# Kernel optimization log

Measured on AMD Instinct MI355X. Metric: run time of the kernel, lower is better.

The kernel has to match this reference:

```python
import jax, jax.numpy as jnp
import numpy as np

B, T, D, H, R = 16, 2048, 512, 1024, 16


def setup_inputs() -> dict:
    key = jax.random.key(0)
    ks = jax.random.split(key, 8)
    s = lambda d: 1.0 / np.sqrt(d)
    return {
        "x": jax.random.normal(ks[0], (B, T, D), jnp.float32),
        "Wx": jax.random.normal(ks[1], (D, H), jnp.float32) * s(D),
        "Wh": jax.random.normal(ks[2], (H, H), jnp.float32) * s(H),
        "Wq": jax.random.normal(ks[3], (D, R), jnp.float32) * s(D),
        "Wk": jax.random.normal(ks[4], (D, R), jnp.float32) * s(D),
        "Wv": jax.random.normal(ks[5], (D, H), jnp.float32) * s(D),
        "Wd": jax.random.normal(ks[6], (D, 1), jnp.float32) * s(D),
        "b": jnp.zeros((H,), jnp.float32),
        "bd": jnp.ones((1,), jnp.float32),
    }


def reference(x, Wx, Wh, Wq, Wk, Wv, Wd, b, bd):
    """DREAM fast-weight RNN.

    Per step: decay lambda_t = sigmoid(x_t Wd + bd)  (B,1)
              F_t = lambda_t * F_{t-1} + v_t k_t^T   (B,H,R) outer-product memory
              r_t = F_t q_t                          (B,H)   fast-weight read
              h_t = tanh(x_t Wx + h_{t-1} Wh + r_t + b)
    """
    Bsz = x.shape[0]
    Hd, Rk = Wv.shape[1], Wq.shape[1]
    # Precompute all time-parallel projections once (big GEMMs outside the scan).
    q = jnp.einsum('btd,dr->btr', x, Wq)            # (B,T,R)
    k = jnp.einsum('btd,dr->btr', x, Wk)            # (B,T,R)
    v = jnp.einsum('btd,dh->bth', x, Wv)            # (B,T,H)
    lam = jax.nn.sigmoid(jnp.einsum('btd,do->bto', x, Wd) + bd)  # (B,T,1)
    xw = jnp.einsum('btd,dh->bth', x, Wx)           # (B,T,H)

    h0 = jnp.zeros((Bsz, Hd), x.dtype)
    F0 = jnp.zeros((Bsz, Hd, Rk), x.dtype)

    def step(carry, inp):
        h, F = carry
        q_t, k_t, v_t, lam_t, xw_t = inp
        F = lam_t[:, :, None] * F + v_t[:, :, None] * k_t[:, None, :]  # (B,H,R)
        read = jnp.einsum('bhr,br->bh', F, q_t)
        h = jnp.tanh(xw_t + h @ Wh + read + b)
        return (h, F), h

    # scan over time axis
    inps = (q.transpose(1, 0, 2), k.transpose(1, 0, 2), v.transpose(1, 0, 2),
            lam.transpose(1, 0, 2), xw.transpose(1, 0, 2))
    (h_fin, F_fin), hs = jax.lax.scan(step, (h0, F0), inps)
    output = hs.transpose(1, 0, 2)  # (B,T,H)
    return output, h_fin, F_fin
```

## Files before the change

### kernel.cpp

```cpp
#include <hip/hip_runtime.h>
#include <math.h>

#define Bc 16
#define Tc 2048
#define Dc 512
#define Hc 1024
#define Rc 16

__global__ __launch_bounds__(256) void proj_fused(const float* __restrict__ X,
    const float* __restrict__ Wx, const float* __restrict__ Wv,
    const float* __restrict__ Wq, const float* __restrict__ Wk,
    const float* __restrict__ Wd, const float* __restrict__ bd,
    float* __restrict__ out0, float* __restrict__ vout,
    float* __restrict__ q, float* __restrict__ k, float* __restrict__ lam)
{
    __shared__ float smem[8192];
    const int tid = threadIdx.x;

    if (blockIdx.z < 2) {
        float (*As)[128] = (float (*)[128])smem;
        float (*Bs)[128] = (float (*)[128])(smem + 2048);
        const float* W = blockIdx.z ? Wv : Wx;
        float* out     = blockIdx.z ? vout : out0;
        const int m0 = blockIdx.x * 128;
        const int n0 = blockIdx.y * 128;
        const int tx = tid & 15, ty = tid >> 4;
        const int ar = tid >> 1, ak = (tid & 1) * 8;
        const int br = tid >> 4, bn = (tid & 15) * 8;
        float acc[8][8] = {};
        for (int k0 = 0; k0 < 512; k0 += 16) {
            if (k0) __syncthreads();
            float4 a0 = *(const float4*)&X[(size_t)(m0 + ar) * 512 + k0 + ak];
            float4 a1 = *(const float4*)&X[(size_t)(m0 + ar) * 512 + k0 + ak + 4];
            float4 b0 = *(const float4*)&W[(size_t)(k0 + br) * 1024 + n0 + bn];
            float4 b1 = *(const float4*)&W[(size_t)(k0 + br) * 1024 + n0 + bn + 4];
            As[ak + 0][ar] = a0.x; As[ak + 1][ar] = a0.y;
            As[ak + 2][ar] = a0.z; As[ak + 3][ar] = a0.w;
            As[ak + 4][ar] = a1.x; As[ak + 5][ar] = a1.y;
            As[ak + 6][ar] = a1.z; As[ak + 7][ar] = a1.w;
            *(float4*)&Bs[br][bn]     = b0;
            *(float4*)&Bs[br][bn + 4] = b1;
            __syncthreads();
            #pragma unroll
            for (int kk = 0; kk < 16; ++kk) {
                float4 xa = *(const float4*)&As[kk][ty * 8];
                float4 xb = *(const float4*)&As[kk][ty * 8 + 4];
                float4 ya = *(const float4*)&Bs[kk][tx * 8];
                float4 yb = *(const float4*)&Bs[kk][tx * 8 + 4];
                float a[8] = {xa.x, xa.y, xa.z, xa.w, xb.x, xb.y, xb.z, xb.w};
                float b[8] = {ya.x, ya.y, ya.z, ya.w, yb.x, yb.y, yb.z, yb.w};
                #pragma unroll
                for (int i = 0; i < 8; ++i)
                    #pragma unroll
                    for (int j = 0; j < 8; ++j)
                        acc[i][j] += a[i] * b[j];
            }
        }
        #pragma unroll
        for (int i = 0; i < 8; ++i) {
            float4 r0, r1;
            r0.x = acc[i][0]; r0.y = acc[i][1]; r0.z = acc[i][2]; r0.w = acc[i][3];
            r1.x = acc[i][4]; r1.y = acc[i][5]; r1.z = acc[i][6]; r1.w = acc[i][7];
            float* op = &out[(size_t)(m0 + ty * 8 + i) * 1024 + n0 + tx * 8];
            *(float4*)op       = r0;
            *(float4*)(op + 4) = r1;
        }
    } else {
        float* xs = smem;
        const int rb = blockIdx.x * 8 + blockIdx.y;
        const size_t row0 = (size_t)rb * 16;
        #pragma unroll
        for (int c = 0; c < 8; ++c) {
            int f = (c * 256 + tid) * 4;
            *(float4*)&xs[f] = *(const float4*)&X[row0 * 512 + f];
        }
        __syncthreads();
        for (int t = tid; t < 528; t += 256) {
            int r = t / 33, c = t - r * 33;
            const float* xr = &xs[r * 512];
            const float* Wp; int ldw;
            if (c < 16)      { Wp = Wq + c;        ldw = 16; }
            else if (c < 32) { Wp = Wk + (c - 16); ldw = 16; }
            else             { Wp = Wd;            ldw = 1;  }
            float s = 0.f;
            for (int kk = 0; kk < 512; ++kk) s += xr[kk] * Wp[(size_t)kk * ldw];
            if (c < 16)      q[(row0 + r) * 16 + c] = s;
            else if (c < 32) k[(row0 + r) * 16 + (c - 16)] = s;
            else             lam[row0 + r] = 1.f / (1.f + expf(-(s + bd[0])));
        }
    }
}

__global__ __launch_bounds__(256, 1) void rec_fused(
    const float* __restrict__ Wh, const float* __restrict__ qg,
    const float* __restrict__ kg, const float* __restrict__ vg,
    const float* __restrict__ lamg, const float* __restrict__ bias,
    float* __restrict__ out0, float* __restrict__ hfin,
    float* __restrict__ Ffin, float* __restrict__ hbuf,
    int* __restrict__ xcc_tab)
{
    __shared__ float hs[2 * 1152];
    __shared__ float red2[2][256];
    __shared__ float pre_lds[2][64];
    __shared__ float F_lds[64][17];

    const int tid = threadIdx.x;
    const int bid = blockIdx.x;
    const int g = bid & 7, sl = bid >> 3;
    const int c0 = sl * 32;
    const int kp = tid >> 3;
    const int cu = tid & 7;
    const int wv = tid >> 6;

    const int my_xcc = __builtin_amdgcn_s_getreg(63508) & 0xF;
    if (tid == 0) {
        int val = my_xcc + 1;
        int* tp = xcc_tab + bid;
        asm volatile("global_store_dword %0, %1, off sc0 sc1"
                     :: "v"(tp), "v"(val) : "memory");
    }

    float wr[128];
    #pragma unroll
    for (int i = 0; i < 32; ++i) {
        float4 w4 = *(const float4*)&Wh[(size_t)(kp * 32 + i) * 1024 + c0 + cu * 4];
        wr[i * 4 + 0] = w4.x; wr[i * 4 + 1] = w4.y;
        wr[i * 4 + 2] = w4.z; wr[i * 4 + 3] = w4.w;
    }

    const int sb_ = tid >> 7;
    const int f   = (tid & 127) * 8;
    float* stage_base = &hs[sb_ * 1152 + (f >> 5) * 36 + (f & 31)];

    int fastf;
    {
        const int prod_bid = (f >> 5) * 8 + g;
        const int* tp = xcc_tab + prod_bid;
        int tv;
        for (;;) {
            asm volatile("global_load_dword %0, %1, off sc0 sc1\n\t"
                         "s_waitcnt vmcnt(0)"
                         : "=&v"(tv) : "v"(tp) : "memory");
            if (tv != -1) break;
        }
        fastf = ((tv - 1) == my_xcc) ? 1 : 0;
    }

    const int j64 = tid & 63;
    const int fb = j64 >> 5, fci = j64 & 31;
    const int bg = g * 2 + fb;
    const bool isScan = (tid >= 192);
    const bool isFin  = (tid < 64);

    float bias_r = 0.f, plam = 0.f, pv = 0.f, pxw = 0.f;
    float4 pq[4], pk4[4];
    if (isScan) {
        bias_r = bias[c0 + fci];
        #pragma unroll
        for (int r = 0; r < 16; ++r) F_lds[j64][r] = 0.f;
        const size_t row = (size_t)bg * Tc;
        plam = lamg[row];
        pv   = vg[row * Hc + c0 + fci];
        pxw  = out0[row * Hc + c0 + fci];
        const float* qp  = qg + row * 16;
        const float* kpp = kg + row * 16;
        #pragma unroll
        for (int r4 = 0; r4 < 4; ++r4) {
            pq[r4]  = *(const float4*)(qp + r4 * 4);
            pk4[r4] = *(const float4*)(kpp + r4 * 4);
        }
    }

    for (int t = 0; t < Tc; ++t) {
        const int buf = t & 1;
        float* h_rd = hbuf + (t & 1) * (16 * 1024) + g * 2048;
        float* h_wr = hbuf + ((t + 1) & 1) * (16 * 1024) + g * 2048;
        const float off_r = ((t >> 1) & 1) ? 4.0f : 0.0f;
        const float off_w = (((t + 1) >> 1) & 1) ? 4.0f : 0.0f;

        if (isScan) {
            float rd = 0.f;
            #pragma unroll
            for (int r4 = 0; r4 < 4; ++r4) {
                float f0 = F_lds[j64][r4 * 4 + 0];
                float f1 = F_lds[j64][r4 * 4 + 1];
                float f2 = F_lds[j64][r4 * 4 + 2];
                float f3 = F_lds[j64][r4 * 4 + 3];
                f0 = plam * f0 + pv * pk4[r4].x; rd += f0 * pq[r4].x;
                f1 = plam * f1 + pv * pk4[r4].y; rd += f1 * pq[r4].y;
                f2 = plam * f2 + pv * pk4[r4].z; rd += f2 * pq[r4].z;
                f3 = plam * f3 + pv * pk4[r4].w; rd += f3 * pq[r4].w;
                F_lds[j64][r4 * 4 + 0] = f0;
                F_lds[j64][r4 * 4 + 1] = f1;
                F_lds[j64][r4 * 4 + 2] = f2;
                F_lds[j64][r4 * 4 + 3] = f3;
            }
            pre_lds[buf][j64] = pxw + rd + bias_r;
            if (t == Tc - 1) {
                #pragma unroll
                for (int r = 0; r < 16; ++r)
                    Ffin[((size_t)bg * Hc + c0 + fci) * 16 + r] = F_lds[j64][r];
            } else {
                const size_t row = (size_t)bg * Tc + (t + 1);
                plam = lamg[row];
                pv   = vg[row * Hc + c0 + fci];
                pxw  = out0[row * Hc + c0 + fci];
                const float* qp  = qg + row * 16;
                const float* kpp = kg + row * 16;
                #pragma unroll
                for (int r4 = 0; r4 < 4; ++r4) {
                    pq[r4]  = *(const float4*)(qp + r4 * 4);
                    pk4[r4] = *(const float4*)(kpp + r4 * 4);
                }
            }
        }

        if (t > 0) {
            const float lo = off_r - 1.5f, hi = off_r + 1.5f;
            const float* p0 = h_rd + sb_ * 1024 + f;
            const float* p1 = p0 + 4;
            float4 r0, r1;
            int tries = 0;
            for (;;) {
                if (fastf) {
                    asm volatile(
                        "global_load_dwordx4 %0, %2, off sc0\n\t"
                        "global_load_dwordx4 %1, %3, off sc0\n\t"
                        "s_waitcnt vmcnt(0)"
                        : "=&v"(r0), "=&v"(r1)
                        : "v"(p0), "v"(p1) : "memory");
                } else {
                    asm volatile(
                        "global_load_dwordx4 %0, %2, off sc0 sc1\n\t"
                        "global_load_dwordx4 %1, %3, off sc0 sc1\n\t"
                        "s_waitcnt vmcnt(0)"
                        : "=&v"(r0), "=&v"(r1)
                        : "v"(p0), "v"(p1) : "memory");
                }
                bool ok = r0.x > lo && r0.x < hi && r0.y > lo && r0.y < hi
                       && r0.z > lo && r0.z < hi && r0.w > lo && r0.w < hi
                       && r1.x > lo && r1.x < hi && r1.y > lo && r1.y < hi
                       && r1.z > lo && r1.z < hi && r1.w > lo && r1.w < hi;
                if (ok) break;
                if (fastf && ++tries > 64) fastf = 0;
            }
            r0.x -= off_r; r0.y -= off_r; r0.z -= off_r; r0.w -= off_r;
            r1.x -= off_r; r1.y -= off_r; r1.z -= off_r; r1.w -= off_r;
            *(float4*)(stage_base)     = r0;
            *(float4*)(stage_base + 4) = r1;
        } else {
            float4 z = {0.f, 0.f, 0.f, 0.f};
            *(float4*)(stage_base)     = z;
            *(float4*)(stage_base + 4) = z;
        }
        __syncthreads();

        float acc[8];
        #pragma unroll
        for (int z = 0; z < 8; ++z) acc[z] = 0.f;
        #pragma unroll
        for (int bb = 0; bb < 2; ++bb) {
            const float* hb = &hs[bb * 1152 + kp * 36];
            #pragma unroll
            for (int i = 0; i < 8; ++i) {
                float4 h4 = *(const float4*)(hb + i * 4);
                #pragma unroll
                for (int j = 0; j < 4; ++j)
                    acc[j * 2 + bb] += h4.x * wr[(i * 4 + 0) * 4 + j]
                                     + h4.y * wr[(i * 4 + 1) * 4 + j]
                                     + h4.z * wr[(i * 4 + 2) * 4 + j]
                                     + h4.w * wr[(i * 4 + 3) * 4 + j];
            }
        }

        #pragma unroll
        for (int z = 0; z < 8; ++z) {
            float s = acc[z];
            s += __shfl_xor(s, 8);
            s += __shfl_xor(s, 16);
            s += __shfl_xor(s, 32);
            acc[z] = s;
        }
        if (j64 < 8) {
            float4 ra, rb;
            ra.x = acc[0]; ra.y = acc[1]; ra.z = acc[2]; ra.w = acc[3];
            rb.x = acc[4]; rb.y = acc[5]; rb.z = acc[6]; rb.w = acc[7];
            *(float4*)&red2[buf][wv * 64 + j64 * 8]     = ra;
            *(float4*)&red2[buf][wv * 64 + j64 * 8 + 4] = rb;
        }
        __syncthreads();

        if (isFin) {
            const int cu_f = fci >> 2, jf = fci & 3;
            const int z = jf * 2 + fb;
            float tot = pre_lds[buf][j64];
            #pragma unroll
            for (int ww = 0; ww < 4; ++ww)
                tot += red2[buf][ww * 64 + cu_f * 8 + z];
            float hv = tanhf(tot);
            float sv = hv + off_w;
            float* hp = h_wr + fb * 1024 + c0 + fci;
            asm volatile(
                "global_store_dword %0, %1, off sc0 sc1"
                :: "v"(hp), "v"(sv) : "memory");
            size_t oidx = ((size_t)bg * Tc + t) * Hc + c0 + fci;
            out0[oidx] = hv;
            if (t == Tc - 1) hfin[(size_t)bg * Hc + c0 + fci] = hv;
        }
    }
}

extern "C" void kernel_launch(void* const* d_in, const int* in_sizes, int n_in,
                              void* d_out, int out_size, void* d_ws, size_t ws_size,
                              hipStream_t stream)
{
    const float* x    = (const float*)d_in[0];
    const float* Wx   = (const float*)d_in[1];
    const float* Wh   = (const float*)d_in[2];
    const float* Wq   = (const float*)d_in[3];
    const float* Wk   = (const float*)d_in[4];
    const float* Wv   = (const float*)d_in[5];
    const float* Wd   = (const float*)d_in[6];
    const float* bias = (const float*)d_in[7];
    const float* bd   = (const float*)d_in[8];

    float* out0 = (float*)d_out;
    float* hfin = out0 + (size_t)Bc * Tc * Hc;
    float* Ffin = hfin + (size_t)Bc * Hc;

    float* wsf  = (float*)d_ws;
    float* v    = wsf;
    float* q    = v + (size_t)Bc * Tc * Hc;
    float* k    = q + (size_t)Bc * Tc * Rc;
    float* lam  = k + (size_t)Bc * Tc * Rc;
    float* hbuf = lam + (size_t)Bc * Tc;
    int*   xcc  = (int*)(hbuf + 2 * (size_t)Bc * Hc);

    hipMemsetAsync(hbuf, 0x7F, 2 * (size_t)Bc * Hc * sizeof(float), stream);
    hipMemsetAsync(xcc, 0xFF, 256 * sizeof(int), stream);

    dim3 gp(256, 8, 3);
    proj_fused<<<gp, 256, 0, stream>>>(x, Wx, Wv, Wq, Wk, Wd, bd,
                                       out0, v, q, k, lam);
    rec_fused<<<256, 256, 0, stream>>>(Wh, q, k, v, lam, bias,
                                       out0, hfin, Ffin, hbuf, xcc);
}
```

Measured before the change: 7.519 ms.

## Fuse projection and recurrence into one persistent kernel with readiness flags

Merges the projection GEMM kernel and the recurrent scan kernel into a single launch. The first 256 blocks run the recurrence, and the remaining blocks compute the projections, publishing per-tile ready flags. Recurrence threads spin on these flags before consuming each 128-step or 16-row chunk, so the scan can start while later projection tiles are still being computed. This removes the launch gap and lets the serial recurrence overlap the GEMM. The risks are deadlock if the recurrence blocks are not all co-resident, less register headroom from launch_bounds(256,2) for the weight-in-register recurrence, and polling overhead.

```diff
diff --git a/kernel.cpp b/kernel.cpp
--- a/kernel.cpp
+++ b/kernel.cpp
@@ -7,105 +7,124 @@
 #define Hc 1024
 #define Rc 16
 
-__global__ __launch_bounds__(256) void proj_fused(const float* __restrict__ X,
+__global__ __launch_bounds__(256, 2) void mega(
+    const float* __restrict__ X,
     const float* __restrict__ Wx, const float* __restrict__ Wv,
     const float* __restrict__ Wq, const float* __restrict__ Wk,
     const float* __restrict__ Wd, const float* __restrict__ bd,
-    float* __restrict__ out0, float* __restrict__ vout,
-    float* __restrict__ q, float* __restrict__ k, float* __restrict__ lam)
+    const float* __restrict__ Wh, const float* __restrict__ bias,
+    float* __restrict__ out0, float* __restrict__ hfin,
+    float* __restrict__ Ffin,
+    float* __restrict__ vg, float* __restrict__ qg, float* __restrict__ kg,
+    float* __restrict__ lamg, float* __restrict__ hbuf,
+    int* __restrict__ xcc_tab,
+    int* __restrict__ fxw, int* __restrict__ fv, int* __restrict__ fqkl)
 {
     __shared__ float smem[8192];
     const int tid = threadIdx.x;
-
-    if (blockIdx.z < 2) {
-        float (*As)[128] = (float (*)[128])smem;
-        float (*Bs)[128] = (float (*)[128])(smem + 2048);
-        const float* W = blockIdx.z ? Wv : Wx;
-        float* out     = blockIdx.z ? vout : out0;
-        const int m0 = blockIdx.x * 128;
-        const int n0 = blockIdx.y * 128;
-        const int tx = tid & 15, ty = tid >> 4;
-        const int ar = tid >> 1, ak = (tid & 1) * 8;
-        const int br = tid >> 4, bn = (tid & 15) * 8;
-        float acc[8][8] = {};
-        for (int k0 = 0; k0 < 512; k0 += 16) {
-            if (k0) __syncthreads();
-            float4 a0 = *(const float4*)&X[(size_t)(m0 + ar) * 512 + k0 + ak];
-            float4 a1 = *(const float4*)&X[(size_t)(m0 + ar) * 512 + k0 + ak + 4];
-            float4 b0 = *(const float4*)&W[(size_t)(k0 + br) * 1024 + n0 + bn];
-            float4 b1 = *(const float4*)&W[(size_t)(k0 + br) * 1024 + n0 + bn + 4];
-            As[ak + 0][ar] = a0.x; As[ak + 1][ar] = a0.y;
-            As[ak + 2][ar] = a0.z; As[ak + 3][ar] = a0.w;
-            As[ak + 4][ar] = a1.x; As[ak + 5][ar] = a1.y;
-            As[ak + 6][ar] = a1.z; As[ak + 7][ar] = a1.w;
-            *(float4*)&Bs[br][bn]     = b0;
-            *(float4*)&Bs[br][bn + 4] = b1;
+    const int bid = blockIdx.x;
+
+    if (bid >= 256) {
+        const int pb = bid - 256;
+        if (pb < 4096) {
+            const int which = pb >> 11;
+            const int idx = pb & 2047;
+            const int mblk = idx >> 3, nblk = idx & 7;
+            float (*As)[128] = (float (*)[128])smem;
+            float (*Bs)[128] = (float (*)[128])(smem + 2048);
+            const float* W = which ? Wv : Wx;
+            float* out     = which ? vg : out0;
+            const int m0 = mblk * 128;
+            const int n0 = nblk * 128;
+            const int tx = tid & 15, ty = tid >> 4;
+            const int ar = tid >> 1, ak = (tid & 1) * 8;
+            const int br = tid >> 4, bn = (tid & 15) * 8;
+            float acc[8][8] = {};
+            for (int k0 = 0; k0 < 512; k0 += 16) {
+                if (k0) __syncthreads();
+                float4 a0 = *(const float4*)&X[(size_t)(m0 + ar) * 512 + k0 + ak];
+                float4 a1 = *(const float4*)&X[(size_t)(m0 + ar) * 512 + k0 + ak + 4];
+                float4 b0 = *(const float4*)&W[(size_t)(k0 + br) * 1024 + n0 + bn];
+                float4 b1 = *(const float4*)&W[(size_t)(k0 + br) * 1024 + n0 + bn + 4];
+                As[ak + 0][ar] = a0.x; As[ak + 1][ar] = a0.y;
+                As[ak + 2][ar] = a0.z; As[ak + 3][ar] = a0.w;
+                As[ak + 4][ar] = a1.x; As[ak + 5][ar] = a1.y;
+                As[ak + 6][ar] = a1.z; As[ak + 7][ar] = a1.w;
+                *(float4*)&Bs[br][bn]     = b0;
+                *(float4*)&Bs[br][bn + 4] = b1;
+                __syncthreads();
+                #pragma unroll
+                for (int kk = 0; kk < 16; ++kk) {
+                    float4 xa = *(const float4*)&As[kk][ty * 8];
+                    float4 xb = *(const float4*)&As[kk][ty * 8 + 4];
+                    float4 ya = *(const float4*)&Bs[kk][tx * 8];
+                    float4 yb = *(const float4*)&Bs[kk][tx * 8 + 4];
+                    float a[8] = {xa.x, xa.y, xa.z, xa.w, xb.x, xb.y, xb.z, xb.w};
+                    float b[8] = {ya.x, ya.y, ya.z, ya.w, yb.x, yb.y, yb.z, yb.w};
+                    #pragma unroll
+                    for (int i = 0; i < 8; ++i)
+                        #pragma unroll
+                        for (int j = 0; j < 8; ++j)
+                            acc[i][j] += a[i] * b[j];
+                }
+            }
+            #pragma unroll
+            for (int i = 0; i < 8; ++i) {
+                float4 r0, r1;
+                r0.x = acc[i][0]; r0.y = acc[i][1]; r0.z = acc[i][2]; r0.w = acc[i][3];
+                r1.x = acc[i][4]; r1.y = acc[i][5]; r1.z = acc[i][6]; r1.w = acc[i][7];
+                float* op = &out[(size_t)(m0 + ty * 8 + i) * 1024 + n0 + tx * 8];
+                *(float4*)op       = r0;
+                *(float4*)(op + 4) = r1;
+            }
             __syncthreads();
+            if (tid == 0) {
+                __builtin_amdgcn_fence(__ATOMIC_RELEASE, "agent");
+                int one = 1;
+                int* fp = (which ? fv : fxw) + idx;
+                asm volatile("global_store_dword %0, %1, off sc0 sc1"
+                             :: "v"(fp), "v"(one) : "memory");
+            }
+        } else {
+            const int rb = pb - 4096;
+            float* xs = smem;
+            const size_t row0 = (size_t)rb * 16;
             #pragma unroll
-            for (int kk = 0; kk < 16; ++kk) {
-                float4 xa = *(const float4*)&As[kk][ty * 8];
-                float4 xb = *(const float4*)&As[kk][ty * 8 + 4];
-                float4 ya = *(const float4*)&Bs[kk][tx * 8];
-                float4 yb = *(const float4*)&Bs[kk][tx * 8 + 4];
-                float a[8] = {xa.x, xa.y, xa.z, xa.w, xb.x, xb.y, xb.z, xb.w};
-                float b[8] = {ya.x, ya.y, ya.z, ya.w, yb.x, yb.y, yb.z, yb.w};
-                #pragma unroll
-                for (int i = 0; i < 8; ++i)
-                    #pragma unroll
-                    for (int j = 0; j < 8; ++j)
-                        acc[i][j] += a[i] * b[j];
-            }
-        }
-        #pragma unroll
-        for (int i = 0; i < 8; ++i) {
-            float4 r0, r1;
-            r0.x = acc[i][0]; r0.y = acc[i][1]; r0.z = acc[i][2]; r0.w = acc[i][3];
-            r1.x = acc[i][4]; r1.y = acc[i][5]; r1.z = acc[i][6]; r1.w = acc[i][7];
-            float* op = &out[(size_t)(m0 + ty * 8 + i) * 1024 + n0 + tx * 8];
-            *(float4*)op       = r0;
-            *(float4*)(op + 4) = r1;
-        }
-    } else {
-        float* xs = smem;
-        const int rb = blockIdx.x * 8 + blockIdx.y;
-        const size_t row0 = (size_t)rb * 16;
-        #pragma unroll
-        for (int c = 0; c < 8; ++c) {
-            int f = (c * 256 + tid) * 4;
-            *(float4*)&xs[f] = *(const float4*)&X[row0 * 512 + f];
-        }
-        __syncthreads();
-        for (int t = tid; t < 528; t += 256) {
-            int r = t / 33, c = t - r * 33;
-            const float* xr = &xs[r * 512];
-            const float* Wp; int ldw;
-            if (c < 16)      { Wp = Wq + c;        ldw = 16; }
-            else if (c < 32) { Wp = Wk + (c - 16); ldw = 16; }
-            else             { Wp = Wd;            ldw = 1;  }
-            float s = 0.f;
-            for (int kk = 0; kk < 512; ++kk) s += xr[kk] * Wp[(size_t)kk * ldw];
-            if (c < 16)      q[(row0 + r) * 16 + c] = s;
-            else if (c < 32) k[(row0 + r) * 16 + (c - 16)] = s;
-            else             lam[row0 + r] = 1.f / (1.f + expf(-(s + bd[0])));
-        }
-    }
-}
-
-__global__ __launch_bounds__(256, 1) void rec_fused(
-    const float* __restrict__ Wh, const float* __restrict__ qg,
-    const float* __restrict__ kg, const float* __restrict__ vg,
-    const float* __restrict__ lamg, const float* __restrict__ bias,
-    float* __restrict__ out0, float* __restrict__ hfin,
-    float* __restrict__ Ffin, float* __restrict__ hbuf,
-    int* __restrict__ xcc_tab)
-{
-    __shared__ float hs[2 * 1152];
-    __shared__ float red2[2][256];
-    __shared__ float pre_lds[2][64];
-    __shared__ float F_lds[64][17];
-
-    const int tid = threadIdx.x;
-    const int bid = blockIdx.x;
+            for (int c = 0; c < 8; ++c) {
+                int f = (c * 256 + tid) * 4;
+                *(float4*)&xs[f] = *(const float4*)&X[row0 * 512 + f];
+            }
+            __syncthreads();
+            for (int t = tid; t < 528; t += 256) {
+                int r = t / 33, c = t - r * 33;
+                const float* xr = &xs[r * 512];
+                const float* Wp; int ldw;
+                if (c < 16)      { Wp = Wq + c;        ldw = 16; }
+                else if (c < 32) { Wp = Wk + (c - 16); ldw = 16; }
+                else             { Wp = Wd;            ldw = 1;  }
+                float s = 0.f;
+                for (int kk = 0; kk < 512; ++kk) s += xr[kk] * Wp[(size_t)kk * ldw];
+                if (c < 16)      qg[(row0 + r) * 16 + c] = s;
+                else if (c < 32) kg[(row0 + r) * 16 + (c - 16)] = s;
+                else             lamg[row0 + r] = 1.f / (1.f + expf(-(s + bd[0])));
+            }
+            __syncthreads();
+            if (tid == 0) {
+                __builtin_amdgcn_fence(__ATOMIC_RELEASE, "agent");
+                int one = 1;
+                int* fp = fqkl + rb;
+                asm volatile("global_store_dword %0, %1, off sc0 sc1"
+                             :: "v"(fp), "v"(one) : "memory");
+            }
+        }
+        return;
+    }
+
+    float* hs       = smem;
+    float* red2     = smem + 2304;
+    float* pre_lds  = smem + 2816;
+    float (*F_lds)[17] = (float (*)[17])(smem + 2944);
+
     const int g = bid & 7, sl = bid >> 3;
     const int c0 = sl * 32;
     const int kp = tid >> 3;
@@ -158,6 +177,31 @@
         bias_r = bias[c0 + fci];
         #pragma unroll
         for (int r = 0; r < 16; ++r) F_lds[j64][r] = 0.f;
+        {
+            const int fidx = (bg * 16 + 0) * 8 + (sl >> 2);
+            int fvv;
+            const int* fp1 = fxw + fidx;
+            for (;;) {
+                asm volatile("global_load_dword %0, %1, off sc0 sc1\n\t"
+                             "s_waitcnt vmcnt(0)" : "=&v"(fvv) : "v"(fp1) : "memory");
+                if (fvv) break;
+                __builtin_amdgcn_s_sleep(8);
+            }
+            const int* fp2 = fv + fidx;
+            for (;;) {
+                asm volatile("global_load_dword %0, %1, off sc0 sc1\n\t"
+                             "s_waitcnt vmcnt(0)" : "=&v"(fvv) : "v"(fp2) : "memory");
+                if (fvv) break;
+                __builtin_amdgcn_s_sleep(8);
+            }
+            const int* fp3 = fqkl + bg * 128;
+            for (;;) {
+                asm volatile("global_load_dword %0, %1, off sc0 sc1\n\t"
+                             "s_waitcnt vmcnt(0)" : "=&v"(fvv) : "v"(fp3) : "memory");
+                if (fvv) break;
+                __builtin_amdgcn_s_sleep(8);
+            }
+        }
         const size_t row = (size_t)bg * Tc;
         plam = lamg[row];
         pv   = vg[row * Hc + c0 + fci];
@@ -195,13 +239,42 @@
                 F_lds[j64][r4 * 4 + 2] = f2;
                 F_lds[j64][r4 * 4 + 3] = f3;
             }
-            pre_lds[buf][j64] = pxw + rd + bias_r;
+            pre_lds[buf * 64 + j64] = pxw + rd + bias_r;
             if (t == Tc - 1) {
                 #pragma unroll
                 for (int r = 0; r < 16; ++r)
                     Ffin[((size_t)bg * Hc + c0 + fci) * 16 + r] = F_lds[j64][r];
             } else {
-                const size_t row = (size_t)bg * Tc + (t + 1);
+                const int trow = t + 1;
+                if ((trow & 127) == 0) {
+                    const int fidx = (bg * 16 + (trow >> 7)) * 8 + (sl >> 2);
+                    int fvv;
+                    const int* fp1 = fxw + fidx;
+                    for (;;) {
+                        asm volatile("global_load_dword %0, %1, off sc0 sc1\n\t"
+                                     "s_waitcnt vmcnt(0)" : "=&v"(fvv) : "v"(fp1) : "memory");
+                        if (fvv) break;
+                        __builtin_amdgcn_s_sleep(8);
+                    }
+                    const int* fp2 = fv + fidx;
+                    for (;;) {
+                        asm volatile("global_load_dword %0, %1, off sc0 sc1\n\t"
+                                     "s_waitcnt vmcnt(0)" : "=&v"(fvv) : "v"(fp2) : "memory");
+                        if (fvv) break;
+                        __builtin_amdgcn_s_sleep(8);
+                    }
+                }
+                if ((trow & 15) == 0) {
+                    int fvv;
+                    const int* fp3 = fqkl + bg * 128 + (trow >> 4);
+                    for (;;) {
+                        asm volatile("global_load_dword %0, %1, off sc0 sc1\n\t"
+                                     "s_waitcnt vmcnt(0)" : "=&v"(fvv) : "v"(fp3) : "memory");
+                        if (fvv) break;
+                        __builtin_amdgcn_s_sleep(8);
+                    }
+                }
+                const size_t row = (size_t)bg * Tc + trow;
                 plam = lamg[row];
                 pv   = vg[row * Hc + c0 + fci];
                 pxw  = out0[row * Hc + c0 + fci];
@@ -285,18 +358,18 @@
             float4 ra, rb;
             ra.x = acc[0]; ra.y = acc[1]; ra.z = acc[2]; ra.w = acc[3];
             rb.x = acc[4]; rb.y = acc[5]; rb.z = acc[6]; rb.w = acc[7];
-            *(float4*)&red2[buf][wv * 64 + j64 * 8]     = ra;
-            *(float4*)&red2[buf][wv * 64 + j64 * 8 + 4] = rb;
+            *(float4*)&red2[buf * 256 + wv * 64 + j64 * 8]     = ra;
+            *(float4*)&red2[buf * 256 + wv * 64 + j64 * 8 + 4] = rb;
         }
         __syncthreads();
 
         if (isFin) {
             const int cu_f = fci >> 2, jf = fci & 3;
             const int z = jf * 2 + fb;
-            float tot = pre_lds[buf][j64];
+            float tot = pre_lds[buf * 64 + j64];
             #pragma unroll
             for (int ww = 0; ww < 4; ++ww)
-                tot += red2[buf][ww * 64 + cu_f * 8 + z];
+                tot += red2[buf * 256 + ww * 64 + cu_f * 8 + z];
             float hv = tanhf(tot);
             float sv = hv + off_w;
             float* hp = h_wr + fb * 1024 + c0 + fci;
@@ -335,13 +408,15 @@
     float* lam  = k + (size_t)Bc * Tc * Rc;
     float* hbuf = lam + (size_t)Bc * Tc;
     int*   xcc  = (int*)(hbuf + 2 * (size_t)Bc * Hc);
+    int*   fxw  = xcc + 256;
+    int*   fvf  = fxw + 2048;
+    int*   fqkl = fvf + 2048;
 
     hipMemsetAsync(hbuf, 0x7F, 2 * (size_t)Bc * Hc * sizeof(float), stream);
     hipMemsetAsync(xcc, 0xFF, 256 * sizeof(int), stream);
-
-    dim3 gp(256, 8, 3);
-    proj_fused<<<gp, 256, 0, stream>>>(x, Wx, Wv, Wq, Wk, Wd, bd,
-                                       out0, v, q, k, lam);
-    rec_fused<<<256, 256, 0, stream>>>(Wh, q, k, v, lam, bias,
-                                       out0, hfin, Ffin, hbuf, xcc);
+    hipMemsetAsync(fxw, 0, 3 * 2048 * sizeof(int), stream);
+
+    mega<<<6400, 256, 0, stream>>>(x, Wx, Wv, Wq, Wk, Wd, bd, Wh, bias,
+                                   out0, hfin, Ffin,
+                                   v, q, k, lam, hbuf, xcc, fxw, fvf, fqkl);
 }
```

New measurement: 14.78 ms. 1.97x slower.
